# Performance work log

Hardware: AMD Instinct MI355X
Metric: run time of the kernel (lower is better)

Reference implementation:

```python
import jax, jax.numpy as jnp
import numpy as np

NUM_HEADS = 8
KERNEL_SEARCH = 5  # local attention window
EPS = 1e-5


def _layernorm(x, g, b):
    m = jnp.mean(x, axis=-1, keepdims=True)
    v = jnp.var(x, axis=-1, keepdims=True)
    return (x - m) / jnp.sqrt(v + EPS) * g + b


def _unfold3(x):
    # x: [N, C, H, W] -> [N, C*9, H*W]; matches torch F.unfold(kernel=3, pad=1)
    # ordering: channel-major, kernel position (row-major) minor.
    N, C, H, W = x.shape
    xp = jnp.pad(x, ((0, 0), (0, 0), (1, 1), (1, 1)))
    pats = jnp.stack([xp[:, :, i:i + H, j:j + W] for i in range(3) for j in range(3)], axis=2)
    return pats.reshape(N, C * 9, H * W)


def _sai2token(x, w_mlp):
    # x: [b, c, a, h, w] -> tokens [h*w, b*a, spa_dim]
    b, c, a, h, w = x.shape
    x = x.transpose(0, 2, 1, 3, 4).reshape(b * a, c, h, w)
    tok = _unfold3(x).transpose(2, 0, 1)  # [hw, b*a, c*9]
    return jnp.einsum('lnk,ek->lne', tok, w_mlp)


def _local_mask(h, w, k):
    # additive mask [h*w, h*w]: 0 inside local kxk window, -inf outside
    kl, kr = k // 2, k - k // 2
    ii = jnp.arange(h)
    jj = jnp.arange(w)
    okh = (ii[None, :] >= ii[:, None] - kl) & (ii[None, :] < ii[:, None] + kr)  # [h,h]
    okw = (jj[None, :] >= jj[:, None] - kl) & (jj[None, :] < jj[:, None] + kr)  # [w,w]
    ok = okh[:, None, :, None] & okw[None, :, None, :]  # [h,w,h,w]
    ok = ok.reshape(h * w, h * w)
    return jnp.where(ok, 0.0, -jnp.inf).astype(jnp.float32)


def _attention(qk_in, v_in, in_proj_w, out_proj_w, bias):
    # qk_in/v_in: [L, B, E]; torch nn.MultiheadAttention, no biases, eval mode
    L, B, E = qk_in.shape
    Dh = E // NUM_HEADS
    Wq, Wk, Wv = in_proj_w[:E], in_proj_w[E:2 * E], in_proj_w[2 * E:]
    q = jnp.einsum('lbe,fe->lbf', qk_in, Wq).reshape(L, B, NUM_HEADS, Dh)
    k = jnp.einsum('lbe,fe->lbf', qk_in, Wk).reshape(L, B, NUM_HEADS, Dh)
    v = jnp.einsum('lbe,fe->lbf', v_in, Wv).reshape(L, B, NUM_HEADS, Dh)
    scale = 1.0 / np.sqrt(Dh).astype(np.float32)
    scores = jnp.einsum('lbhd,mbhd->bhlm', q, k) * scale + bias[None, None]
    attn = jax.nn.softmax(scores, axis=-1)
    out = jnp.einsum('bhlm,mbhd->lbhd', attn, v).reshape(L, B, E)
    return jnp.einsum('lbe,fe->lbf', out, out_proj_w)


def reference(buffer, spa_position, w_mlp, ln1_g, ln1_b, in_proj_w, out_proj_w,
              ln2_g, ln2_b, ff_w1, ff_w2, conv_w):
    b, c, a, h, w = buffer.shape
    bias = _local_mask(h, w, KERNEL_SEARCH)
    tok = _sai2token(buffer, w_mlp)          # [hw, b*a, E]
    pe = _sai2token(spa_position, w_mlp)
    x = _layernorm(tok + pe, ln1_g, ln1_b)
    tok = _attention(x, tok, in_proj_w, out_proj_w, bias) + tok
    # feed-forward (dropout is identity in eval)
    ff = _layernorm(tok, ln2_g, ln2_b)
    ff = jax.nn.relu(jnp.einsum('lbe,fe->lbf', ff, ff_w1))
    tok = jnp.einsum('lbf,ef->lbe', ff, ff_w2) + tok
    # Token2SAI: '(h w) (b a) e -> b e a h w' then 1x1x1 conv3d
    buf = tok.reshape(h, w, b, a, -1).transpose(2, 4, 3, 0, 1)  # [b, E, a, h, w]
    return jnp.einsum('oe,beahw->boahw', conv_w, buf)


def setup_inputs() -> dict:
    key = jax.random.key(0)
    ks = jax.random.split(key, 8)
    b, c, a, h, w = 1, 64, 25, 32, 32
    E = 2 * c
    s = 0.02
    return {
        'buffer': jax.random.normal(ks[0], (b, c, a, h, w), jnp.float32),
        'spa_position': jax.random.normal(ks[1], (b, c, a, h, w), jnp.float32),
        'w_mlp': jax.random.normal(ks[2], (E, c * 9), jnp.float32) * s,
        'ln1_g': jnp.ones((E,), jnp.float32),
        'ln1_b': jnp.zeros((E,), jnp.float32),
        'in_proj_w': jax.random.normal(ks[3], (3 * E, E), jnp.float32) * s,
        'out_proj_w': jax.random.normal(ks[4], (E, E), jnp.float32) * s,
        'ln2_g': jnp.ones((E,), jnp.float32),
        'ln2_b': jnp.zeros((E,), jnp.float32),
        'ff_w1': jax.random.normal(ks[5], (2 * E, E), jnp.float32) * s,
        'ff_w2': jax.random.normal(ks[6], (E, 2 * E), jnp.float32) * s,
        'conv_w': jax.random.normal(ks[7], (c, E), jnp.float32) * s,
    }
```

## Files before the change

### kernel.cpp

```cpp
#include <hip/hip_runtime.h>
#include <hip/hip_bf16.h>
#include <math.h>

#define Lh 32
#define Lw 32
#define LL 1024
#define BN 25
#define EE 128
#define CC 64
#define NHD 8
#define DH 16
#define FFD 256
#define MROWS 25600

typedef __attribute__((ext_vector_type(8))) short short8;
typedef __attribute__((ext_vector_type(4))) float f32x4;

__device__ inline ushort f2b(float x) {
    union { float f; unsigned u; } v; v.f = x;
    unsigned r = (v.u + 0x7fffu + ((v.u >> 16) & 1u)) >> 16;
    return (ushort)r;
}
__device__ inline unsigned pk2(float a, float b) {
    union { __hip_bfloat162 h; unsigned u; } c;
    c.h = __float22bfloat162_rn(make_float2(a, b));
    return c.u;
}
__device__ inline float b2f(ushort u) {
    union { unsigned u; float f; } v; v.u = ((unsigned)u) << 16;
    return v.f;
}

#define OFF_W2  0
#define OFF_WQK 73728
#define OFF_WV  106496
#define OFF_WO  122880
#define OFF_W1  139264
#define OFF_W2F 172032
#define OFF_WC  204800
#define W_TOTAL 212992

__global__ __launch_bounds__(256) void k_prep(
    const float* __restrict__ w_mlp, const float* __restrict__ in_proj,
    const float* __restrict__ out_proj, const float* __restrict__ ff_w1,
    const float* __restrict__ ff_w2, const float* __restrict__ conv_w,
    ushort* __restrict__ Wb)
{
    int i = blockIdx.x * 256 + threadIdx.x;
    if (i >= W_TOTAL) return;
    if (i < 73728) {
        int e = i / 576, k = i - e * 576;
        int tap = k >> 6, ch = k & 63;
        Wb[OFF_W2 + i] = f2b(w_mlp[e * 576 + ch * 9 + tap]);
        return;
    }
    i -= 73728;
    if (i < 32768) {
        float v = in_proj[i];
        Wb[OFF_WQK + i] = f2b(i < 16384 ? v * 0.25f : v);
        return;
    }
    i -= 32768;
    if (i < 16384) { Wb[OFF_WV + i] = f2b(in_proj[32768 + i]); return; }
    i -= 16384;
    if (i < 16384) {
        int e = i >> 7, kpos = i & 127;
        int c = kpos >> 5, q = (kpos >> 3) & 3, ii = kpos & 7;
        int orig = (2 * c + (ii >> 2)) * 16 + q * 4 + (ii & 3);
        Wb[OFF_WO + i] = f2b(out_proj[e * 128 + orig]);
        return;
    }
    i -= 16384;
    if (i < 32768) { Wb[OFF_W1 + i] = f2b(ff_w1[i]); return; }
    i -= 32768;
    if (i < 32768) {
        int e = i >> 8, kpos = i & 255;
        int c = kpos >> 5, q = (kpos >> 3) & 3, ii = kpos & 7;
        int orig = (2 * c + (ii >> 2)) * 16 + q * 4 + (ii & 3);
        Wb[OFF_W2F + i] = f2b(ff_w2[e * 256 + orig]);
        return;
    }
    i -= 32768;
    {
        int o = i >> 7, kpos = i & 127;
        int c = kpos >> 5, q = (kpos >> 3) & 3, ii = kpos & 7;
        int orig = (2 * c + (ii >> 2)) * 16 + q * 4 + (ii & 3);
        Wb[OFF_WC + i] = f2b(conv_w[o * 128 + orig]);
    }
}

__global__ __launch_bounds__(256, 3) void k_tok_qkv(
    const float* __restrict__ buf, const float* __restrict__ spa,
    const ushort* __restrict__ W2, const ushort* __restrict__ WQK,
    const ushort* __restrict__ WV, const float* __restrict__ g1,
    const float* __restrict__ b1, ushort* __restrict__ TOKb,
    ushort* __restrict__ Qh, ushort* __restrict__ Kh, ushort* __restrict__ VTg)
{
    const int bid = blockIdx.x;
    const int idx = (bid & 7) * 100 + (bid >> 3);
    const int n = idx / 32, y = idx & 31;
    __shared__ ushort At[3 * 34 * 72];
    __shared__ ushort As_[3 * 34 * 72];
    __shared__ ushort Xs[32 * 136];
    __shared__ ushort Vs[32 * 136];
    __shared__ float2 red[32][4];
    float* t0 = (float*)Xs;
    float* t1 = (float*)Vs;
    const int t = threadIdx.x;
    const uint4 z = make_uint4(0, 0, 0, 0);

    for (int dy = 0; dy < 3; dy++) {
        int yy = y + dy - 1;
        if (yy >= 0 && yy < Lh) {
            {
                int ch = t >> 2, x8 = (t & 3) * 8;
                const float* p = buf + ((size_t)(ch * BN + n) * LL + yy * Lw + x8);
                const float* q = spa + ((size_t)(ch * BN + n) * LL + yy * Lw + x8);
                float4 a0 = ((const float4*)p)[0], a1 = ((const float4*)p)[1];
                float4 b0 = ((const float4*)q)[0], b1 = ((const float4*)q)[1];
                float* d0 = t0 + ch * 33 + x8;
                float* d1 = t1 + ch * 33 + x8;
                d0[0] = a0.x; d0[1] = a0.y; d0[2] = a0.z; d0[3] = a0.w;
                d0[4] = a1.x; d0[5] = a1.y; d0[6] = a1.z; d0[7] = a1.w;
                d1[0] = a0.x + b0.x; d1[1] = a0.y + b0.y; d1[2] = a0.z + b0.z; d1[3] = a0.w + b0.w;
                d1[4] = a1.x + b1.x; d1[5] = a1.y + b1.y; d1[6] = a1.z + b1.z; d1[7] = a1.w + b1.w;
            }
            __syncthreads();
            {
                int x = t >> 3, c8 = (t & 7) * 8;
                union { unsigned u[4]; uint4 v; } o0, o1;
#pragma unroll
                for (int j = 0; j < 4; j++) {
                    o0.u[j] = pk2(t0[(c8 + 2 * j) * 33 + x], t0[(c8 + 2 * j + 1) * 33 + x]);
                    o1.u[j] = pk2(t1[(c8 + 2 * j) * 33 + x], t1[(c8 + 2 * j + 1) * 33 + x]);
                }
                *(uint4*)(At + (dy * 34 + x + 1) * 72 + c8) = o0.v;
                *(uint4*)(As_ + (dy * 34 + x + 1) * 72 + c8) = o1.v;
            }
            __syncthreads();
        } else {
            int x = t >> 3, c8 = (t & 7) * 8;
            *(uint4*)(At + (dy * 34 + x + 1) * 72 + c8) = z;
            *(uint4*)(As_ + (dy * 34 + x + 1) * 72 + c8) = z;
        }
    }
    if (t < 48) {
        int dy = t / 16, rem = t % 16;
        int colp = (rem >> 3) * 33, c8p = (rem & 7) * 8;
        *(uint4*)(At + (dy * 34 + colp) * 72 + c8p) = z;
        *(uint4*)(As_ + (dy * 34 + colp) * 72 + c8p) = z;
    }
    __syncthreads();

    const int w = t >> 6, lane = t & 63;
    const int col = lane & 15, quad = lane >> 4;
    f32x4 accT[2][2] = {}, accS[2][2] = {};

    for (int tap = 0; tap < 9; tap++) {
        int dy = tap / 3, dx = tap % 3;
#pragma unroll
        for (int cc = 0; cc < 2; cc++) {
            int kg = tap * 64 + cc * 32 + quad * 8;
            short8 b0 = *(const short8*)(W2 + (size_t)(w * 32 + col) * 576 + kg);
            short8 bq = *(const short8*)(W2 + (size_t)(w * 32 + 16 + col) * 576 + kg);
            int abase = (dy * 34 + col + dx) * 72 + cc * 32 + quad * 8;
            short8 aT0 = *(const short8*)(At + abase);
            short8 aT1 = *(const short8*)(At + abase + 16 * 72);
            short8 aS0 = *(const short8*)(As_ + abase);
            short8 aS1 = *(const short8*)(As_ + abase + 16 * 72);
            accT[0][0] = __builtin_amdgcn_mfma_f32_16x16x32_bf16(aT0, b0, accT[0][0], 0, 0, 0);
            accT[0][1] = __builtin_amdgcn_mfma_f32_16x16x32_bf16(aT0, bq, accT[0][1], 0, 0, 0);
            accT[1][0] = __builtin_amdgcn_mfma_f32_16x16x32_bf16(aT1, b0, accT[1][0], 0, 0, 0);
            accT[1][1] = __builtin_amdgcn_mfma_f32_16x16x32_bf16(aT1, bq, accT[1][1], 0, 0, 0);
            accS[0][0] = __builtin_amdgcn_mfma_f32_16x16x32_bf16(aS0, b0, accS[0][0], 0, 0, 0);
            accS[0][1] = __builtin_amdgcn_mfma_f32_16x16x32_bf16(aS0, bq, accS[0][1], 0, 0, 0);
            accS[1][0] = __builtin_amdgcn_mfma_f32_16x16x32_bf16(aS1, b0, accS[1][0], 0, 0, 0);
            accS[1][1] = __builtin_amdgcn_mfma_f32_16x16x32_bf16(aS1, bq, accS[1][1], 0, 0, 0);
        }
    }

#pragma unroll
    for (int mi = 0; mi < 2; mi++)
#pragma unroll
        for (int r = 0; r < 4; r++) {
            float a0 = accS[mi][0][r], a1 = accS[mi][1][r];
            float ss = a0 + a1, qq = a0 * a0 + a1 * a1;
#pragma unroll
            for (int m = 1; m < 16; m <<= 1) {
                ss += __shfl_xor(ss, m, 64);
                qq += __shfl_xor(qq, m, 64);
            }
            if (col == 0) red[mi * 16 + quad * 4 + r][w] = make_float2(ss, qq);
        }
    __syncthreads();

    const float ga = g1[w * 32 + col],      ba = b1[w * 32 + col];
    const float gb = g1[w * 32 + 16 + col], bb = b1[w * 32 + 16 + col];
#pragma unroll
    for (int mi = 0; mi < 2; mi++)
#pragma unroll
        for (int r = 0; r < 4; r++) {
            int x = mi * 16 + quad * 4 + r;
            float2 p0 = red[x][0], p1 = red[x][1], p2 = red[x][2], p3 = red[x][3];
            float mean = (p0.x + p1.x + p2.x + p3.x) * (1.f / 128.f);
            float var  = (p0.y + p1.y + p2.y + p3.y) * (1.f / 128.f) - mean * mean;
            float rstd = rsqrtf(var + 1e-5f);
            int e0 = w * 32 + col, e1 = w * 32 + 16 + col;
            Xs[x * 136 + e0] = f2b((accS[mi][0][r] - mean) * rstd * ga + ba);
            Xs[x * 136 + e1] = f2b((accS[mi][1][r] - mean) * rstd * gb + bb);
            Vs[x * 136 + e0] = f2b(accT[mi][0][r]);
            Vs[x * 136 + e1] = f2b(accT[mi][1][r]);
        }
    __syncthreads();

    short8 xb[2][4], xv[2][4];
#pragma unroll
    for (int j = 0; j < 2; j++)
#pragma unroll
        for (int kc = 0; kc < 4; kc++) {
            xb[j][kc] = *(const short8*)(Xs + (j * 16 + col) * 136 + kc * 32 + quad * 8);
            xv[j][kc] = *(const short8*)(Vs + (j * 16 + col) * 136 + kc * 32 + quad * 8);
        }
    f32x4 Q[2][2] = {}, K[2][2] = {}, V[2][2] = {};
#pragma unroll
    for (int hj = 0; hj < 2; hj++) {
        int h = 2 * w + hj;
#pragma unroll
        for (int kc = 0; kc < 4; kc++) {
            short8 aq = *(const short8*)(WQK + (size_t)(h * 16 + col) * 128 + kc * 32 + quad * 8);
            short8 ak = *(const short8*)(WQK + (size_t)(128 + h * 16 + col) * 128 + kc * 32 + quad * 8);
            short8 av = *(const short8*)(WV + (size_t)(h * 16 + col) * 128 + kc * 32 + quad * 8);
#pragma unroll
            for (int j = 0; j < 2; j++) {
                Q[hj][j] = __builtin_amdgcn_mfma_f32_16x16x32_bf16(aq, xb[j][kc], Q[hj][j], 0, 0, 0);
                K[hj][j] = __builtin_amdgcn_mfma_f32_16x16x32_bf16(ak, xb[j][kc], K[hj][j], 0, 0, 0);
                V[hj][j] = __builtin_amdgcn_mfma_f32_16x16x32_bf16(av, xv[j][kc], V[hj][j], 0, 0, 0);
            }
        }
    }
    ushort* VTs = At;
#pragma unroll
    for (int hj = 0; hj < 2; hj++) {
        int h = 2 * w + hj;
#pragma unroll
        for (int j = 0; j < 2; j++) {
            int l = y * 32 + j * 16 + col;
            size_t base = ((size_t)(n * 8 + h) * 1024 + l) * 16 + quad * 4;
            union { unsigned u[2]; uint2 v; } oq, ok;
            oq.u[0] = pk2(Q[hj][j][0], Q[hj][j][1]); oq.u[1] = pk2(Q[hj][j][2], Q[hj][j][3]);
            ok.u[0] = pk2(K[hj][j][0], K[hj][j][1]); ok.u[1] = pk2(K[hj][j][2], K[hj][j][3]);
            *(uint2*)(Qh + base) = oq.v;
            *(uint2*)(Kh + base) = ok.v;
            int xp = ((col >> 2) << 3) + (j << 2) + (col & 3);
#pragma unroll
            for (int r = 0; r < 4; r++)
                VTs[(h * 16 + quad * 4 + r) * 34 + xp] = f2b(V[hj][j][r]);
        }
    }
#pragma unroll
    for (int k = 0; k < 2; k++) {
        int idx2 = t + k * 256;
        int r = idx2 >> 4, seg = idx2 & 15;
        *(uint4*)(TOKb + ((size_t)((y * 32 + r) * 25 + n)) * 128 + seg * 8) =
            *(const uint4*)(Vs + r * 136 + seg * 8);
    }
    __syncthreads();
    {
        int h = t >> 5, rem = t & 31, d = rem >> 1, xh = (rem & 1) * 16;
        size_t vrow = ((size_t)(n * 8 + h) * 32 + y) * 512;
        union { ushort u[8]; uint4 v; } o0, o1;
#pragma unroll
        for (int j = 0; j < 8; j++) {
            o0.u[j] = VTs[(h * 16 + d) * 34 + xh + j];
            o1.u[j] = VTs[(h * 16 + d) * 34 + xh + 8 + j];
        }
        *(uint4*)(VTg + vrow + d * 32 + xh)     = o0.v;
        *(uint4*)(VTg + vrow + d * 32 + xh + 8) = o1.v;
    }
}

__global__ __launch_bounds__(256, 4) void k_attn_ffn(
    const ushort* __restrict__ Qh, const ushort* __restrict__ Kh,
    const ushort* __restrict__ VTg, const ushort* __restrict__ WOP,
    const float* __restrict__ g2, const float* __restrict__ b2,
    const ushort* __restrict__ W1, const ushort* __restrict__ W2P,
    const ushort* __restrict__ WCP, const ushort* __restrict__ TOKb,
    float* __restrict__ out)
{
    __shared__ ushort OX[16 * 136];
    __shared__ ushort Rs[16 * 136];
    __shared__ ushort Hs[16 * 264];
    __shared__ float2 red[16][4];
    ushort* Ys = Rs;
    const int bid = blockIdx.x;
    const int idx = (bid & 7) * 200 + (bid >> 3);
    const int n = idx / 64, rem = idx & 63;
    const int y = rem >> 1, half = rem & 1;
    const int l0 = y * 32 + half * 16;
    const int t = threadIdx.x, w = t >> 6, lane = t & 63;
    const int col = lane & 15, quad = lane >> 4;
    const int qx = half * 16 + col;

    {
        int r = t >> 4, seg = t & 15;
        *(uint4*)(Rs + r * 136 + seg * 8) =
            *(const uint4*)(TOKb + ((size_t)((l0 + r) * 25 + n)) * 128 + seg * 8);
    }

    unsigned long long mbits = 0;
#pragma unroll
    for (int tt = 0; tt < 10; tt++) {
        int yy = y - 2 + (tt >> 1);
        bool rok = (yy >= 0) && (yy < 32);
        int kxb = ((tt & 1) << 4) + quad * 4;
#pragma unroll
        for (int r = 0; r < 4; r++) {
            int dd = kxb + r - qx;
            if (rok && ((unsigned)(dd + 2) <= 4u))
                mbits |= 1ull << (tt * 4 + r);
        }
    }

    short8 z8 = {0, 0, 0, 0, 0, 0, 0, 0};
    f32x4 O2[2] = {};
#pragma unroll
    for (int hj = 0; hj < 2; hj++) {
        const int h = 2 * w + hj;
        const size_t base = (size_t)(n * 8 + h) * 1024;
        const size_t vbase = (size_t)(n * 8 + h) * 32 * 512;

        short8 qf = z8;
        if (quad < 2)
            qf = *(const short8*)(Qh + (base + y * 32 + half * 16 + col) * 16 + quad * 8);

        f32x4 Sc[10] = {};
#pragma unroll
        for (int tt = 0; tt < 10; tt++) {
            int kr = tt >> 1, kx = ((tt & 1) << 4) + col;
            int yyc = min(max(y - 2 + kr, 0), 31);
            short8 kf = z8;
            if (quad < 2)
                kf = *(const short8*)(Kh + (base + yyc * 32 + kx) * 16 + quad * 8);
            Sc[tt] = __builtin_amdgcn_mfma_f32_16x16x32_bf16(kf, qf, Sc[tt], 0, 0, 0);
        }

        float sum = 0.f;
#pragma unroll
        for (int tt = 0; tt < 10; tt++)
#pragma unroll
            for (int r = 0; r < 4; r++) {
                bool ok = (mbits >> (tt * 4 + r)) & 1;
                float p = ok ? __expf(Sc[tt][r]) : 0.f;
                Sc[tt][r] = p;
                sum += p;
            }
        sum += __shfl_xor(sum, 16, 64);
        sum += __shfl_xor(sum, 32, 64);
        const float inv = 1.f / sum;

#pragma unroll
        for (int c = 0; c < 5; c++) {
            int yyc = min(max(y - 2 + c, 0), 31);
            short8 vt = *(const short8*)(VTg + vbase + (size_t)yyc * 512 + col * 32 + quad * 8);
            union { unsigned u[4]; short8 s; } pb;
            pb.u[0] = pk2(Sc[2 * c][0], Sc[2 * c][1]);
            pb.u[1] = pk2(Sc[2 * c][2], Sc[2 * c][3]);
            pb.u[2] = pk2(Sc[2 * c + 1][0], Sc[2 * c + 1][1]);
            pb.u[3] = pk2(Sc[2 * c + 1][2], Sc[2 * c + 1][3]);
            O2[hj] = __builtin_amdgcn_mfma_f32_16x16x32_bf16(vt, pb.s, O2[hj], 0, 0, 0);
        }
#pragma unroll
        for (int r = 0; r < 4; r++) O2[hj][r] *= inv;
    }

    {
        union { unsigned u[4]; uint4 v; } pb;
        pb.u[0] = pk2(O2[0][0], O2[0][1]); pb.u[1] = pk2(O2[0][2], O2[0][3]);
        pb.u[2] = pk2(O2[1][0], O2[1][1]); pb.u[3] = pk2(O2[1][2], O2[1][3]);
        *(uint4*)(OX + col * 136 + w * 32 + quad * 8) = pb.v;
    }
    __syncthreads();

    f32x4 Y[2] = {};
#pragma unroll
    for (int kc = 0; kc < 4; kc++) {
        short8 hb = *(const short8*)(OX + col * 136 + kc * 32 + quad * 8);
#pragma unroll
        for (int jj = 0; jj < 2; jj++) {
            int et = 2 * w + jj;
            short8 a = *(const short8*)(WOP + (size_t)(et * 16 + col) * 128 + kc * 32 + quad * 8);
            Y[jj] = __builtin_amdgcn_mfma_f32_16x16x32_bf16(a, hb, Y[jj], 0, 0, 0);
        }
    }
    float sum = 0.f, sq = 0.f;
#pragma unroll
    for (int jj = 0; jj < 2; jj++)
#pragma unroll
        for (int r = 0; r < 4; r++) {
            int e = (2 * w + jj) * 16 + quad * 4 + r;
            float v = Y[jj][r] + b2f(Rs[col * 136 + e]);
            Y[jj][r] = v;
            sum += v; sq += v * v;
        }
    sum += __shfl_xor(sum, 16, 64); sum += __shfl_xor(sum, 32, 64);
    sq  += __shfl_xor(sq, 16, 64);  sq  += __shfl_xor(sq, 32, 64);
    if (quad == 0) red[col][w] = make_float2(sum, sq);
    __syncthreads();

    {
        float2 p0 = red[col][0], p1 = red[col][1], p2 = red[col][2], p3 = red[col][3];
        float mean = (p0.x + p1.x + p2.x + p3.x) * (1.f / 128.f);
        float var  = (p0.y + p1.y + p2.y + p3.y) * (1.f / 128.f) - mean * mean;
        float rstd = rsqrtf(var + 1e-5f);
#pragma unroll
        for (int jj = 0; jj < 2; jj++)
#pragma unroll
            for (int r2 = 0; r2 < 4; r2 += 2) {
                int e = (2 * w + jj) * 16 + quad * 4 + r2;
                float v0 = (Y[jj][r2]     - mean) * rstd * g2[e]     + b2[e];
                float v1 = (Y[jj][r2 + 1] - mean) * rstd * g2[e + 1] + b2[e + 1];
                *(unsigned*)(OX + col * 136 + e) = pk2(v0, v1);
            }
    }
    __syncthreads();

    short8 xb[4];
#pragma unroll
    for (int kc = 0; kc < 4; kc++)
        xb[kc] = *(const short8*)(OX + col * 136 + kc * 32 + quad * 8);
    f32x4 H[4] = {};
#pragma unroll
    for (int j = 0; j < 4; j++) {
        int ft = 4 * w + j;
#pragma unroll
        for (int kc = 0; kc < 4; kc++) {
            short8 a = *(const short8*)(W1 + (size_t)(ft * 16 + col) * 128 + kc * 32 + quad * 8);
            H[j] = __builtin_amdgcn_mfma_f32_16x16x32_bf16(a, xb[kc], H[j], 0, 0, 0);
        }
    }
#pragma unroll
    for (int cc = 0; cc < 2; cc++) {
        union { unsigned u[4]; uint4 v; } pb;
        pb.u[0] = pk2(fmaxf(H[2 * cc][0], 0.f), fmaxf(H[2 * cc][1], 0.f));
        pb.u[1] = pk2(fmaxf(H[2 * cc][2], 0.f), fmaxf(H[2 * cc][3], 0.f));
        pb.u[2] = pk2(fmaxf(H[2 * cc + 1][0], 0.f), fmaxf(H[2 * cc + 1][1], 0.f));
        pb.u[3] = pk2(fmaxf(H[2 * cc + 1][2], 0.f), fmaxf(H[2 * cc + 1][3], 0.f));
        *(uint4*)(Hs + col * 264 + (2 * w + cc) * 32 + quad * 8) = pb.v;
    }
    __syncthreads();

    f32x4 Y2[2] = {};
#pragma unroll
    for (int kc = 0; kc < 8; kc++) {
        short8 hb = *(const short8*)(Hs + col * 264 + kc * 32 + quad * 8);
#pragma unroll
        for (int j = 0; j < 2; j++) {
            int et = 2 * w + j;
            short8 a = *(const short8*)(W2P + (size_t)(et * 16 + col) * 256 + kc * 32 + quad * 8);
            Y2[j] = __builtin_amdgcn_mfma_f32_16x16x32_bf16(a, hb, Y2[j], 0, 0, 0);
        }
    }
    {
        union { unsigned u[4]; uint4 v; } pb;
        pb.u[0] = pk2(Y2[0][0] + Y[0][0], Y2[0][1] + Y[0][1]);
        pb.u[1] = pk2(Y2[0][2] + Y[0][2], Y2[0][3] + Y[0][3]);
        pb.u[2] = pk2(Y2[1][0] + Y[1][0], Y2[1][1] + Y[1][1]);
        pb.u[3] = pk2(Y2[1][2] + Y[1][2], Y2[1][3] + Y[1][3]);
        *(uint4*)(Ys + col * 136 + w * 32 + quad * 8) = pb.v;
    }
    __syncthreads();

    f32x4 O = {};
#pragma unroll
    for (int c = 0; c < 4; c++) {
        short8 yb = *(const short8*)(Ys + col * 136 + c * 32 + quad * 8);
        short8 a = *(const short8*)(WCP + (size_t)(w * 16 + col) * 128 + c * 32 + quad * 8);
        O = __builtin_amdgcn_mfma_f32_16x16x32_bf16(a, yb, O, 0, 0, 0);
    }
    const int l = l0 + col;
#pragma unroll
    for (int r2 = 0; r2 < 4; r2++) {
        int o = w * 16 + quad * 4 + r2;
        out[(size_t)(o * 25 + n) * 1024 + l] = O[r2];
    }
}

extern "C" void kernel_launch(void* const* d_in, const int* in_sizes, int n_in,
                              void* d_out, int out_size, void* d_ws, size_t ws_size,
                              hipStream_t stream)
{
    const float* buffer   = (const float*)d_in[0];
    const float* spa      = (const float*)d_in[1];
    const float* w_mlp    = (const float*)d_in[2];
    const float* ln1_g    = (const float*)d_in[3];
    const float* ln1_b    = (const float*)d_in[4];
    const float* in_proj  = (const float*)d_in[5];
    const float* out_proj = (const float*)d_in[6];
    const float* ln2_g    = (const float*)d_in[7];
    const float* ln2_b    = (const float*)d_in[8];
    const float* ff_w1    = (const float*)d_in[9];
    const float* ff_w2    = (const float*)d_in[10];
    const float* conv_w   = (const float*)d_in[11];
    float* out = (float*)d_out;

    char* ws = (char*)d_ws;
    ushort* TOKb = (ushort*)(ws);
    ushort* Qh   = (ushort*)(ws + 6553600);
    ushort* Kh   = (ushort*)(ws + 13107200);
    ushort* VTg  = (ushort*)(ws + 19660800);
    ushort* Wb   = (ushort*)(ws + 26214400);

    k_prep<<<dim3((W_TOTAL + 255) / 256), 256, 0, stream>>>(
        w_mlp, in_proj, out_proj, ff_w1, ff_w2, conv_w, Wb);
    k_tok_qkv<<<dim3(800), 256, 0, stream>>>(buffer, spa, Wb + OFF_W2,
                                             Wb + OFF_WQK, Wb + OFF_WV,
                                             ln1_g, ln1_b, TOKb, Qh, Kh, VTg);
    k_attn_ffn<<<dim3(1600), 256, 0, stream>>>(Qh, Kh, VTg, Wb + OFF_WO,
                                               ln2_g, ln2_b, Wb + OFF_W1,
                                               Wb + OFF_W2F, Wb + OFF_WC,
                                               TOKb, out);
}
```

Baseline: 174.1 us.

## Split attention-FFN block work across eight waves, one head per wave

Result: no change. 173.2 us (-0.5%).

```diff
diff --git a/kernel.cpp b/kernel.cpp
--- a/kernel.cpp
+++ b/kernel.cpp
@@ -279,7 +279,8 @@
     }
 }
 
-__global__ __launch_bounds__(256, 4) void k_attn_ffn(
+__global__ __launch_bounds__(512)
+void k_attn_ffn(
     const ushort* __restrict__ Qh, const ushort* __restrict__ Kh,
     const ushort* __restrict__ VTg, const ushort* __restrict__ WOP,
     const float* __restrict__ g2, const float* __restrict__ b2,
@@ -290,7 +291,7 @@
     __shared__ ushort OX[16 * 136];
     __shared__ ushort Rs[16 * 136];
     __shared__ ushort Hs[16 * 264];
-    __shared__ float2 red[16][4];
+    __shared__ float2 red[16][8];
     ushort* Ys = Rs;
     const int bid = blockIdx.x;
     const int idx = (bid & 7) * 200 + (bid >> 3);
@@ -302,9 +303,9 @@
     const int qx = half * 16 + col;
 
     {
-        int r = t >> 4, seg = t & 15;
-        *(uint4*)(Rs + r * 136 + seg * 8) =
-            *(const uint4*)(TOKb + ((size_t)((l0 + r) * 25 + n)) * 128 + seg * 8);
+        int r = t >> 5, seg = t & 31;
+        *(uint2*)(Rs + r * 136 + seg * 4) =
+            *(const uint2*)(TOKb + ((size_t)((l0 + r) * 25 + n)) * 128 + seg * 4);
     }
 
     unsigned long long mbits = 0;
@@ -322,105 +323,95 @@
     }
 
     short8 z8 = {0, 0, 0, 0, 0, 0, 0, 0};
-    f32x4 O2[2] = {};
-#pragma unroll
-    for (int hj = 0; hj < 2; hj++) {
-        const int h = 2 * w + hj;
-        const size_t base = (size_t)(n * 8 + h) * 1024;
-        const size_t vbase = (size_t)(n * 8 + h) * 32 * 512;
-
-        short8 qf = z8;
+    const size_t base = (size_t)(n * 8 + w) * 1024;
+    const size_t vbase = (size_t)(n * 8 + w) * 32 * 512;
+
+    short8 qf = z8;
+    if (quad < 2)
+        qf = *(const short8*)(Qh + (base + y * 32 + half * 16 + col) * 16 + quad * 8);
+
+    f32x4 Sc[10] = {};
+#pragma unroll
+    for (int tt = 0; tt < 10; tt++) {
+        int kr = tt >> 1, kx = ((tt & 1) << 4) + col;
+        int yyc = min(max(y - 2 + kr, 0), 31);
+        short8 kf = z8;
         if (quad < 2)
-            qf = *(const short8*)(Qh + (base + y * 32 + half * 16 + col) * 16 + quad * 8);
-
-        f32x4 Sc[10] = {};
-#pragma unroll
-        for (int tt = 0; tt < 10; tt++) {
-            int kr = tt >> 1, kx = ((tt & 1) << 4) + col;
-            int yyc = min(max(y - 2 + kr, 0), 31);
-            short8 kf = z8;
-            if (quad < 2)
-                kf = *(const short8*)(Kh + (base + yyc * 32 + kx) * 16 + quad * 8);
-            Sc[tt] = __builtin_amdgcn_mfma_f32_16x16x32_bf16(kf, qf, Sc[tt], 0, 0, 0);
-        }
-
-        float sum = 0.f;
-#pragma unroll
-        for (int tt = 0; tt < 10; tt++)
-#pragma unroll
-            for (int r = 0; r < 4; r++) {
-                bool ok = (mbits >> (tt * 4 + r)) & 1;
-                float p = ok ? __expf(Sc[tt][r]) : 0.f;
-                Sc[tt][r] = p;
-                sum += p;
-            }
-        sum += __shfl_xor(sum, 16, 64);
-        sum += __shfl_xor(sum, 32, 64);
-        const float inv = 1.f / sum;
-
-#pragma unroll
-        for (int c = 0; c < 5; c++) {
-            int yyc = min(max(y - 2 + c, 0), 31);
-            short8 vt = *(const short8*)(VTg + vbase + (size_t)yyc * 512 + col * 32 + quad * 8);
-            union { unsigned u[4]; short8 s; } pb;
-            pb.u[0] = pk2(Sc[2 * c][0], Sc[2 * c][1]);
-            pb.u[1] = pk2(Sc[2 * c][2], Sc[2 * c][3]);
-            pb.u[2] = pk2(Sc[2 * c + 1][0], Sc[2 * c + 1][1]);
-            pb.u[3] = pk2(Sc[2 * c + 1][2], Sc[2 * c + 1][3]);
-            O2[hj] = __builtin_amdgcn_mfma_f32_16x16x32_bf16(vt, pb.s, O2[hj], 0, 0, 0);
-        }
-#pragma unroll
-        for (int r = 0; r < 4; r++) O2[hj][r] *= inv;
-    }
-
-    {
-        union { unsigned u[4]; uint4 v; } pb;
-        pb.u[0] = pk2(O2[0][0], O2[0][1]); pb.u[1] = pk2(O2[0][2], O2[0][3]);
-        pb.u[2] = pk2(O2[1][0], O2[1][1]); pb.u[3] = pk2(O2[1][2], O2[1][3]);
-        *(uint4*)(OX + col * 136 + w * 32 + quad * 8) = pb.v;
-    }
-    __syncthreads();
-
-    f32x4 Y[2] = {};
+            kf = *(const short8*)(Kh + (base + yyc * 32 + kx) * 16 + quad * 8);
+        Sc[tt] = __builtin_amdgcn_mfma_f32_16x16x32_bf16(kf, qf, Sc[tt], 0, 0, 0);
+    }
+
+    float sum = 0.f;
+#pragma unroll
+    for (int tt = 0; tt < 10; tt++)
+#pragma unroll
+        for (int r = 0; r < 4; r++) {
+            bool ok = (mbits >> (tt * 4 + r)) & 1;
+            float p = ok ? __expf(Sc[tt][r]) : 0.f;
+            Sc[tt][r] = p;
+            sum += p;
+        }
+    sum += __shfl_xor(sum, 16, 64);
+    sum += __shfl_xor(sum, 32, 64);
+    const float inv = 1.f / sum;
+
+    f32x4 O2 = {};
+#pragma unroll
+    for (int c = 0; c < 5; c++) {
+        int yyc = min(max(y - 2 + c, 0), 31);
+        short8 vt = *(const short8*)(VTg + vbase + (size_t)yyc * 512 + col * 32 + quad * 8);
+        union { unsigned u[4]; short8 s; } pb;
+        pb.u[0] = pk2(Sc[2 * c][0], Sc[2 * c][1]);
+        pb.u[1] = pk2(Sc[2 * c][2], Sc[2 * c][3]);
+        pb.u[2] = pk2(Sc[2 * c + 1][0], Sc[2 * c + 1][1]);
+        pb.u[3] = pk2(Sc[2 * c + 1][2], Sc[2 * c + 1][3]);
+        O2 = __builtin_amdgcn_mfma_f32_16x16x32_bf16(vt, pb.s, O2, 0, 0, 0);
+    }
+#pragma unroll
+    for (int r = 0; r < 4; r++) O2[r] *= inv;
+
+    {
+        union { unsigned u[2]; uint2 v; } pb;
+        pb.u[0] = pk2(O2[0], O2[1]);
+        pb.u[1] = pk2(O2[2], O2[3]);
+        *(uint2*)(OX + col * 136 + (w >> 1) * 32 + quad * 8 + (w & 1) * 4) = pb.v;
+    }
+    __syncthreads();
+
+    f32x4 Y = {};
 #pragma unroll
     for (int kc = 0; kc < 4; kc++) {
         short8 hb = *(const short8*)(OX + col * 136 + kc * 32 + quad * 8);
-#pragma unroll
-        for (int jj = 0; jj < 2; jj++) {
-            int et = 2 * w + jj;
-            short8 a = *(const short8*)(WOP + (size_t)(et * 16 + col) * 128 + kc * 32 + quad * 8);
-            Y[jj] = __builtin_amdgcn_mfma_f32_16x16x32_bf16(a, hb, Y[jj], 0, 0, 0);
-        }
-    }
-    float sum = 0.f, sq = 0.f;
-#pragma unroll
-    for (int jj = 0; jj < 2; jj++)
-#pragma unroll
-        for (int r = 0; r < 4; r++) {
-            int e = (2 * w + jj) * 16 + quad * 4 + r;
-            float v = Y[jj][r] + b2f(Rs[col * 136 + e]);
-            Y[jj][r] = v;
-            sum += v; sq += v * v;
-        }
-    sum += __shfl_xor(sum, 16, 64); sum += __shfl_xor(sum, 32, 64);
-    sq  += __shfl_xor(sq, 16, 64);  sq  += __shfl_xor(sq, 32, 64);
-    if (quad == 0) red[col][w] = make_float2(sum, sq);
-    __syncthreads();
-
-    {
-        float2 p0 = red[col][0], p1 = red[col][1], p2 = red[col][2], p3 = red[col][3];
-        float mean = (p0.x + p1.x + p2.x + p3.x) * (1.f / 128.f);
-        float var  = (p0.y + p1.y + p2.y + p3.y) * (1.f / 128.f) - mean * mean;
+        short8 a = *(const short8*)(WOP + (size_t)(w * 16 + col) * 128 + kc * 32 + quad * 8);
+        Y = __builtin_amdgcn_mfma_f32_16x16x32_bf16(a, hb, Y, 0, 0, 0);
+    }
+    float s2 = 0.f, q2 = 0.f;
+#pragma unroll
+    for (int r = 0; r < 4; r++) {
+        int e = w * 16 + quad * 4 + r;
+        float v = Y[r] + b2f(Rs[col * 136 + e]);
+        Y[r] = v;
+        s2 += v; q2 += v * v;
+    }
+    s2 += __shfl_xor(s2, 16, 64); s2 += __shfl_xor(s2, 32, 64);
+    q2 += __shfl_xor(q2, 16, 64); q2 += __shfl_xor(q2, 32, 64);
+    if (quad == 0) red[col][w] = make_float2(s2, q2);
+    __syncthreads();
+
+    {
+        float s = 0.f, q = 0.f;
+#pragma unroll
+        for (int j = 0; j < 8; j++) { s += red[col][j].x; q += red[col][j].y; }
+        float mean = s * (1.f / 128.f);
+        float var  = q * (1.f / 128.f) - mean * mean;
         float rstd = rsqrtf(var + 1e-5f);
 #pragma unroll
-        for (int jj = 0; jj < 2; jj++)
-#pragma unroll
-            for (int r2 = 0; r2 < 4; r2 += 2) {
-                int e = (2 * w + jj) * 16 + quad * 4 + r2;
-                float v0 = (Y[jj][r2]     - mean) * rstd * g2[e]     + b2[e];
-                float v1 = (Y[jj][r2 + 1] - mean) * rstd * g2[e + 1] + b2[e + 1];
-                *(unsigned*)(OX + col * 136 + e) = pk2(v0, v1);
-            }
+        for (int r2 = 0; r2 < 4; r2 += 2) {
+            int e = w * 16 + quad * 4 + r2;
+            float v0 = (Y[r2]     - mean) * rstd * g2[e]     + b2[e];
+            float v1 = (Y[r2 + 1] - mean) * rstd * g2[e + 1] + b2[e + 1];
+            *(unsigned*)(OX + col * 136 + e) = pk2(v0, v1);
+        }
     }
     __syncthreads();
 
@@ -428,60 +419,55 @@
 #pragma unroll
     for (int kc = 0; kc < 4; kc++)
         xb[kc] = *(const short8*)(OX + col * 136 + kc * 32 + quad * 8);
-    f32x4 H[4] = {};
-#pragma unroll
-    for (int j = 0; j < 4; j++) {
-        int ft = 4 * w + j;
+    f32x4 H[2] = {};
+#pragma unroll
+    for (int jj = 0; jj < 2; jj++) {
+        int ft = 2 * w + jj;
 #pragma unroll
         for (int kc = 0; kc < 4; kc++) {
             short8 a = *(const short8*)(W1 + (size_t)(ft * 16 + col) * 128 + kc * 32 + quad * 8);
-            H[j] = __builtin_amdgcn_mfma_f32_16x16x32_bf16(a, xb[kc], H[j], 0, 0, 0);
-        }
-    }
-#pragma unroll
-    for (int cc = 0; cc < 2; cc++) {
+            H[jj] = __builtin_amdgcn_mfma_f32_16x16x32_bf16(a, xb[kc], H[jj], 0, 0, 0);
+        }
+    }
+    {
         union { unsigned u[4]; uint4 v; } pb;
-        pb.u[0] = pk2(fmaxf(H[2 * cc][0], 0.f), fmaxf(H[2 * cc][1], 0.f));
-        pb.u[1] = pk2(fmaxf(H[2 * cc][2], 0.f), fmaxf(H[2 * cc][3], 0.f));
-        pb.u[2] = pk2(fmaxf(H[2 * cc + 1][0], 0.f), fmaxf(H[2 * cc + 1][1], 0.f));
-        pb.u[3] = pk2(fmaxf(H[2 * cc + 1][2], 0.f), fmaxf(H[2 * cc + 1][3], 0.f));
-        *(uint4*)(Hs + col * 264 + (2 * w + cc) * 32 + quad * 8) = pb.v;
-    }
-    __syncthreads();
-
-    f32x4 Y2[2] = {};
+        pb.u[0] = pk2(fmaxf(H[0][0], 0.f), fmaxf(H[0][1], 0.f));
+        pb.u[1] = pk2(fmaxf(H[0][2], 0.f), fmaxf(H[0][3], 0.f));
+        pb.u[2] = pk2(fmaxf(H[1][0], 0.f), fmaxf(H[1][1], 0.f));
+        pb.u[3] = pk2(fmaxf(H[1][2], 0.f), fmaxf(H[1][3], 0.f));
+        *(uint4*)(Hs + col * 264 + w * 32 + quad * 8) = pb.v;
+    }
+    __syncthreads();
+
+    f32x4 Y2 = {};
 #pragma unroll
     for (int kc = 0; kc < 8; kc++) {
         short8 hb = *(const short8*)(Hs + col * 264 + kc * 32 + quad * 8);
-#pragma unroll
-        for (int j = 0; j < 2; j++) {
-            int et = 2 * w + j;
-            short8 a = *(const short8*)(W2P + (size_t)(et * 16 + col) * 256 + kc * 32 + quad * 8);
-            Y2[j] = __builtin_amdgcn_mfma_f32_16x16x32_bf16(a, hb, Y2[j], 0, 0, 0);
-        }
-    }
-    {
-        union { unsigned u[4]; uint4 v; } pb;
-        pb.u[0] = pk2(Y2[0][0] + Y[0][0], Y2[0][1] + Y[0][1]);
-        pb.u[1] = pk2(Y2[0][2] + Y[0][2], Y2[0][3] + Y[0][3]);
-        pb.u[2] = pk2(Y2[1][0] + Y[1][0], Y2[1][1] + Y[1][1]);
-        pb.u[3] = pk2(Y2[1][2] + Y[1][2], Y2[1][3] + Y[1][3]);
-        *(uint4*)(Ys + col * 136 + w * 32 + quad * 8) = pb.v;
-    }
-    __syncthreads();
-
-    f32x4 O = {};
-#pragma unroll
-    for (int c = 0; c < 4; c++) {
-        short8 yb = *(const short8*)(Ys + col * 136 + c * 32 + quad * 8);
-        short8 a = *(const short8*)(WCP + (size_t)(w * 16 + col) * 128 + c * 32 + quad * 8);
-        O = __builtin_amdgcn_mfma_f32_16x16x32_bf16(a, yb, O, 0, 0, 0);
-    }
-    const int l = l0 + col;
-#pragma unroll
-    for (int r2 = 0; r2 < 4; r2++) {
-        int o = w * 16 + quad * 4 + r2;
-        out[(size_t)(o * 25 + n) * 1024 + l] = O[r2];
+        short8 a = *(const short8*)(W2P + (size_t)(w * 16 + col) * 256 + kc * 32 + quad * 8);
+        Y2 = __builtin_amdgcn_mfma_f32_16x16x32_bf16(a, hb, Y2, 0, 0, 0);
+    }
+    {
+        union { unsigned u[2]; uint2 v; } pb;
+        pb.u[0] = pk2(Y2[0] + Y[0], Y2[1] + Y[1]);
+        pb.u[1] = pk2(Y2[2] + Y[2], Y2[3] + Y[3]);
+        *(uint2*)(Ys + col * 136 + (w >> 1) * 32 + quad * 8 + (w & 1) * 4) = pb.v;
+    }
+    __syncthreads();
+
+    if (w < 4) {
+        f32x4 O = {};
+#pragma unroll
+        for (int c = 0; c < 4; c++) {
+            short8 yb = *(const short8*)(Ys + col * 136 + c * 32 + quad * 8);
+            short8 a = *(const short8*)(WCP + (size_t)(w * 16 + col) * 128 + c * 32 + quad * 8);
+            O = __builtin_amdgcn_mfma_f32_16x16x32_bf16(a, yb, O, 0, 0, 0);
+        }
+        const int l = l0 + col;
+#pragma unroll
+        for (int r2 = 0; r2 < 4; r2++) {
+            int o = w * 16 + quad * 4 + r2;
+            out[(size_t)(o * 25 + n) * 1024 + l] = O[r2];
+        }
     }
 }
 
@@ -515,7 +501,7 @@
     k_tok_qkv<<<dim3(800), 256, 0, stream>>>(buffer, spa, Wb + OFF_W2,
                                              Wb + OFF_WQK, Wb + OFF_WV,
                                              ln1_g, ln1_b, TOKb, Qh, Kh, VTg);
-    k_attn_ffn<<<dim3(1600), 256, 0, stream>>>(Qh, Kh, VTg, Wb + OFF_WO,
+    k_attn_ffn<<<dim3(1600), 512, 0, stream>>>(Qh, Kh, VTg, Wb + OFF_WO,
                                                ln2_g, ln2_b, Wb + OFF_W1,
                                                Wb + OFF_W2F, Wb + OFF_WC,
                                                TOKb, out);
```
